# Kernel tuning notes

Hardware: AMD Instinct MI355X
Metric: run time of the kernel (lower is better)

The kernel has to match this reference:

```python
import jax, jax.numpy as jnp
import numpy as np

V, E = 100000, 128   # vocab, embed_size
B, S, N = 32, 1024, 16  # batch, seq_len, n_negatives


def setup_inputs() -> dict:
    key = jax.random.key(0)
    k1, k2, k3, k4 = jax.random.split(key, 4)
    sentence = jax.random.randint(k1, (B, S), 0, V, dtype=jnp.int64)
    context = jax.random.normal(k2, (B, S, E), dtype=jnp.float32)
    # WalkerAlias negative sampling happens on CPU in the original; here the
    # sampled indices are precomputed inputs (uniform counter ** power -> uniform).
    neg_samples = jax.random.randint(k3, (B, S, N), 0, V, dtype=jnp.int64)
    W = jax.random.normal(k4, (V, E), dtype=jnp.float32) * 0.02
    return {"sentence": sentence, "context": context, "neg_samples": neg_samples, "W": W}


def reference(sentence, context, neg_samples, W):
    emb = W[sentence]                                   # [B,S,E] gather
    pos_loss = jax.nn.log_sigmoid(jnp.sum(emb * context, axis=-1))          # [B,S]
    neg_emb = W[neg_samples]                            # [B,S,N,E] gather
    neg_scores = jnp.einsum('bsne,bse->bsn', neg_emb, context)              # [B,S,N]
    neg_loss = jnp.sum(jax.nn.log_sigmoid(-neg_scores), axis=-1)            # [B,S]
    return -jnp.sum(pos_loss + neg_loss)
```

## Files before the change

kernel.cpp:

```cpp
#include <hip/hip_runtime.h>
#include <hip/hip_bf16.h>
#include <cmath>

#define NS_ROWS   32768u
#define NS_PAIRS  (NS_ROWS * 17u)
#define NS_BLOCKS 8704

__device__ __forceinline__ float log_sigmoid_f(float x) {
    return fminf(x, 0.0f) - log1pf(__expf(-fabsf(x)));
}

__global__ __launch_bounds__(256) void ns_main_kernel(
    const int*   __restrict__ sentence,
    const float* __restrict__ context,
    const int*   __restrict__ neg,
    const float* __restrict__ W,
    float*       __restrict__ partial)
{
    const int tid = threadIdx.x;
    const int l   = tid & 31;
    const unsigned g = blockIdx.x * 8u + (unsigned)(tid >> 5);
    const unsigned p0 = g * 8u;

    unsigned r0 = p0 / 17u, t0 = p0 - r0 * 17u;
    int idx = (t0 == 0u) ? sentence[r0] : neg[(r0 << 4) + (t0 - 1u)];

    float loss = 0.0f;
#pragma unroll
    for (int i = 0; i < 8; ++i) {
        const unsigned p    = p0 + (unsigned)i;
        const unsigned prow = p / 17u;
        const unsigned ptgt = p - prow * 17u;
        const int cur = idx;

        if (i < 7) {
            const unsigned pn = p + 1u;
            const unsigned nr = pn / 17u, nt = pn - nr * 17u;
            idx = (nt == 0u) ? sentence[nr] : neg[(nr << 4) + (nt - 1u)];
        }

        const float4 wv = *reinterpret_cast<const float4*>(W + ((size_t)cur << 7) + (l << 2));
        const float4 cv = *reinterpret_cast<const float4*>(context + ((size_t)prow << 7) + (l << 2));
        float acc = wv.x * cv.x + wv.y * cv.y + wv.z * cv.z + wv.w * cv.w;

        acc += __shfl_xor(acc, 1,  64);
        acc += __shfl_xor(acc, 2,  64);
        acc += __shfl_xor(acc, 4,  64);
        acc += __shfl_xor(acc, 8,  64);
        acc += __shfl_xor(acc, 16, 64);

        loss += log_sigmoid_f((ptgt == 0u) ? acc : -acc);
    }
    loss *= (1.0f / 32.0f);

    loss = loss * 32.0f;
    loss = ((l == 0) ? loss : 0.0f);
    loss += __shfl_xor(loss, 32, 64);
#pragma unroll
    for (int m = 16; m >= 1; m >>= 1) loss += __shfl_xor(loss, m, 64);

    __shared__ float wsum[4];
    const int wave = tid >> 6, lane = tid & 63;
    if (lane == 0) wsum[wave] = loss;
    __syncthreads();
    if (tid == 0) partial[blockIdx.x] = wsum[0] + wsum[1] + wsum[2] + wsum[3];
}

__global__ __launch_bounds__(1024) void ns_reduce_kernel(
    const float* __restrict__ partial, float* __restrict__ out)
{
    const int tid = threadIdx.x;
    float s = 0.0f;
    for (int i = tid; i < NS_BLOCKS; i += 1024) s += partial[i];
#pragma unroll
    for (int m = 32; m >= 1; m >>= 1) s += __shfl_xor(s, m, 64);

    __shared__ float wsum[16];
    const int wave = tid >> 6, lane = tid & 63;
    if (lane == 0) wsum[wave] = s;
    __syncthreads();
    if (tid == 0) {
        float t = 0.0f;
#pragma unroll
        for (int i = 0; i < 16; ++i) t += wsum[i];
        out[0] = -t;
    }
}

extern "C" void kernel_launch(void* const* d_in, const int* in_sizes, int n_in,
                              void* d_out, int out_size, void* d_ws, size_t ws_size,
                              hipStream_t stream) {
    const int*   sentence = (const int*)d_in[0];
    const float* context  = (const float*)d_in[1];
    const int*   neg      = (const int*)d_in[2];
    const float* W        = (const float*)d_in[3];
    float*       out      = (float*)d_out;
    float*       partial  = (float*)d_ws;

    ns_main_kernel<<<NS_BLOCKS, 256, 0, stream>>>(sentence, context, neg, W, partial);
    ns_reduce_kernel<<<1, 1024, 0, stream>>>(partial, out);
}
```

Measured before the change: 62.38 us.

## Map one pair per 16-lane group with 1024-thread blocks, dropping serial loop

Each (row, target) pair is now handled by 16 lanes that each load two float4s of the W row and the context row, where before 32 lanes looped serially over 8 pairs with index prefetching. Blocks grow to 1024 threads covering 64 pairs each, so the same block count still covers all pairs, and the per-block reduction now sums 16 wave partials. The goal is more memory-level parallelism and less per-thread loop and index arithmetic. The cost is more threads and more shuffle reductions per pair, and the context row is reloaded separately for each of its 17 pairs rather than reused within one thread's loop.

```diff
diff --git a/kernel.cpp b/kernel.cpp
--- a/kernel.cpp
+++ b/kernel.cpp
@@ -10,7 +10,11 @@
     return fminf(x, 0.0f) - log1pf(__expf(-fabsf(x)));
 }
 
-__global__ __launch_bounds__(256) void ns_main_kernel(
+__device__ __forceinline__ float dot4(const float4 a, const float4 b) {
+    return a.x * b.x + a.y * b.y + a.z * b.z + a.w * b.w;
+}
+
+__global__ __launch_bounds__(1024) void ns_main_kernel(
     const int*   __restrict__ sentence,
     const float* __restrict__ context,
     const int*   __restrict__ neg,
@@ -18,52 +22,44 @@
     float*       __restrict__ partial)
 {
     const int tid = threadIdx.x;
-    const int l   = tid & 31;
-    const unsigned g = blockIdx.x * 8u + (unsigned)(tid >> 5);
-    const unsigned p0 = g * 8u;
+    const int m   = tid & 15;
+    const unsigned pair = (blockIdx.x << 6) | (unsigned)(tid >> 4);
 
-    unsigned r0 = p0 / 17u, t0 = p0 - r0 * 17u;
-    int idx = (t0 == 0u) ? sentence[r0] : neg[(r0 << 4) + (t0 - 1u)];
+    const unsigned row = pair / 17u;
+    const unsigned tgt = pair - row * 17u;
 
-    float loss = 0.0f;
+    const float* cb = context + ((size_t)row << 7) + (m << 3);
+    const float4 c0 = *reinterpret_cast<const float4*>(cb);
+    const float4 c1 = *reinterpret_cast<const float4*>(cb + 4);
+
+    const int idx = (tgt == 0u) ? sentence[row] : neg[(row << 4) + (tgt - 1u)];
+
+    const float* wb = W + ((size_t)idx << 7) + (m << 3);
+    const float4 w0 = *reinterpret_cast<const float4*>(wb);
+    const float4 w1 = *reinterpret_cast<const float4*>(wb + 4);
+
+    float acc = dot4(w0, c0) + dot4(w1, c1);
+
+    acc += __shfl_xor(acc, 1, 64);
+    acc += __shfl_xor(acc, 2, 64);
+    acc += __shfl_xor(acc, 4, 64);
+    acc += __shfl_xor(acc, 8, 64);
+
+    float loss = (m == 0) ? log_sigmoid_f((tgt == 0u) ? acc : -acc) : 0.0f;
+
 #pragma unroll
-    for (int i = 0; i < 8; ++i) {
-        const unsigned p    = p0 + (unsigned)i;
-        const unsigned prow = p / 17u;
-        const unsigned ptgt = p - prow * 17u;
-        const int cur = idx;
+    for (int s = 32; s >= 1; s >>= 1) loss += __shfl_xor(loss, s, 64);
 
-        if (i < 7) {
-            const unsigned pn = p + 1u;
-            const unsigned nr = pn / 17u, nt = pn - nr * 17u;
-            idx = (nt == 0u) ? sentence[nr] : neg[(nr << 4) + (nt - 1u)];
-        }
-
-        const float4 wv = *reinterpret_cast<const float4*>(W + ((size_t)cur << 7) + (l << 2));
-        const float4 cv = *reinterpret_cast<const float4*>(context + ((size_t)prow << 7) + (l << 2));
-        float acc = wv.x * cv.x + wv.y * cv.y + wv.z * cv.z + wv.w * cv.w;
-
-        acc += __shfl_xor(acc, 1,  64);
-        acc += __shfl_xor(acc, 2,  64);
-        acc += __shfl_xor(acc, 4,  64);
-        acc += __shfl_xor(acc, 8,  64);
-        acc += __shfl_xor(acc, 16, 64);
-
-        loss += log_sigmoid_f((ptgt == 0u) ? acc : -acc);
-    }
-    loss *= (1.0f / 32.0f);
-
-    loss = loss * 32.0f;
-    loss = ((l == 0) ? loss : 0.0f);
-    loss += __shfl_xor(loss, 32, 64);
-#pragma unroll
-    for (int m = 16; m >= 1; m >>= 1) loss += __shfl_xor(loss, m, 64);
-
-    __shared__ float wsum[4];
+    __shared__ float wsum[16];
     const int wave = tid >> 6, lane = tid & 63;
     if (lane == 0) wsum[wave] = loss;
     __syncthreads();
-    if (tid == 0) partial[blockIdx.x] = wsum[0] + wsum[1] + wsum[2] + wsum[3];
+    if (tid == 0) {
+        float t = 0.0f;
+#pragma unroll
+        for (int i = 0; i < 16; ++i) t += wsum[i];
+        partial[blockIdx.x] = t;
+    }
 }
 
 __global__ __launch_bounds__(1024) void ns_reduce_kernel(
@@ -97,6 +93,6 @@
     float*       out      = (float*)d_out;
     float*       partial  = (float*)d_ws;
 
-    ns_main_kernel<<<NS_BLOCKS, 256, 0, stream>>>(sentence, context, neg, W, partial);
+    ns_main_kernel<<<NS_BLOCKS, 1024, 0, stream>>>(sentence, context, neg, W, partial);
     ns_reduce_kernel<<<1, 1024, 0, stream>>>(partial, out);
 }
```

Measured after the change: 56.77 us. 9.0% less time.
